# Kernel optimization log

Hardware: AMD Instinct MI355X
Metric: run time of the kernel (lower is better)

Reference implementation:

```python
import jax, jax.numpy as jnp
import numpy as np

D = 512       # d_model
DC = 768      # d_context
H = 8         # heads
DFF = 2048    # d_ff
EPS = 1e-6


def _ln(x, g, b):
    mu = jnp.mean(x, axis=-1, keepdims=True)
    var = jnp.mean(jnp.square(x - mu), axis=-1, keepdims=True)
    return (x - mu) * jax.lax.rsqrt(var + EPS) * g + b


def _mha(q_in, k_in, v_in, mask, wq, bq, wk, bk, wv, bv, wo, bo):
    # q_in [B,Sq,D], k_in/v_in [B,Sk,D], mask [B,Sq,Sk] (nonzero -> blocked)
    B, Sq, _ = q_in.shape
    Sk = k_in.shape[1]
    dh = D // H
    q = (q_in @ wq + bq).reshape(B, Sq, H, dh)
    k = (k_in @ wk + bk).reshape(B, Sk, H, dh)
    v = (v_in @ wv + bv).reshape(B, Sk, H, dh)
    scores = jnp.einsum('bqhd,bkhd->bhqk', q, k) / np.float32(np.sqrt(dh))
    scores = jnp.where(mask[:, None, :, :].astype(bool), jnp.float32(-1e18), scores)
    attn = jax.nn.softmax(scores, axis=-1)
    ctx = jnp.einsum('bhqk,bkhd->bqhd', attn, v).reshape(B, Sq, D)
    return ctx @ wo + bo


def _aggregate_chains(batch_size, ctx_out, chain_map, chain_mask):
    # ctx_out [TC,S,D]; keep positions where mask[:,:,0] is set, else -inf,
    # then max-pool chains belonging to the same example (segment max).
    keep = chain_mask[:, :, 0].astype(bool)[:, :, None]
    masked = jnp.where(keep, ctx_out, jnp.float32(-jnp.inf))
    out = jax.ops.segment_max(masked, chain_map, num_segments=batch_size)
    # replicate torch.where(out + 1 == out, 0, out): zeros out -inf entries
    return jnp.where(out + 1 == out, jnp.float32(0.0), out)


def _lin_params(key, din, dout):
    return jax.random.normal(key, (din, dout), jnp.float32) * 0.02, jnp.zeros((dout,), jnp.float32)


def setup_inputs() -> dict:
    key = jax.random.key(0)
    ks = jax.random.split(key, 20)
    B, S, TC, L = 16, 512, 128, 12
    inp = {}
    inp['inputs'] = jax.random.normal(ks[0], (B, S, D), jnp.float32)
    inp['attn_mask'] = jax.random.randint(ks[1], (B, S, S), 0, 2, jnp.int32)
    inp['chain_map'] = jax.random.randint(ks[2], (TC,), 0, B, jnp.int32)
    inp['span_embeddings'] = jax.random.normal(ks[3], (TC, L, DC), jnp.float32)
    inp['chain_mask'] = jax.random.randint(ks[4], (TC, S, L), 0, 2, jnp.int32)
    inp['ln_g'] = jnp.ones((D,), jnp.float32)
    inp['ln_b'] = jnp.zeros((D,), jnp.float32)
    inp['sa_wq'], inp['sa_bq'] = _lin_params(ks[5], D, D)
    inp['sa_wk'], inp['sa_bk'] = _lin_params(ks[6], D, D)
    inp['sa_wv'], inp['sa_bv'] = _lin_params(ks[7], D, D)
    inp['sa_wo'], inp['sa_bo'] = _lin_params(ks[8], D, D)
    inp['lc_w'], inp['lc_b'] = _lin_params(ks[9], DC, D)
    inp['ca_wq'], inp['ca_bq'] = _lin_params(ks[10], D, D)
    inp['ca_wk'], inp['ca_bk'] = _lin_params(ks[11], D, D)
    inp['ca_wv'], inp['ca_bv'] = _lin_params(ks[12], D, D)
    inp['ca_wo'], inp['ca_bo'] = _lin_params(ks[13], D, D)
    inp['g_w'], inp['g_b'] = _lin_params(ks[14], 2 * D, D)
    inp['ff_ln_g'] = jnp.ones((D,), jnp.float32)
    inp['ff_ln_b'] = jnp.zeros((D,), jnp.float32)
    inp['ff_w1'], inp['ff_b1'] = _lin_params(ks[15], D, DFF)
    inp['ff_w2'], inp['ff_b2'] = _lin_params(ks[16], DFF, D)
    return inp


def reference(inputs, attn_mask, chain_map, span_embeddings, chain_mask,
              ln_g, ln_b,
              sa_wq, sa_bq, sa_wk, sa_bk, sa_wv, sa_bv, sa_wo, sa_bo,
              lc_w, lc_b,
              ca_wq, ca_bq, ca_wk, ca_bk, ca_wv, ca_bv, ca_wo, ca_bo,
              g_w, g_b,
              ff_ln_g, ff_ln_b, ff_w1, ff_b1, ff_w2, ff_b2):
    B = inputs.shape[0]
    input_norm = _ln(inputs, ln_g, ln_b)
    attn_context = _mha(input_norm, input_norm, input_norm, attn_mask,
                        sa_wq, sa_bq, sa_wk, sa_bk, sa_wv, sa_bv, sa_wo, sa_bo)
    emb_transformed = span_embeddings @ lc_w + lc_b              # [TC,L,D]
    context_query = input_norm[chain_map]                         # [TC,S,D]
    ctx_out = _mha(context_query, emb_transformed, emb_transformed, chain_mask,
                   ca_wq, ca_bq, ca_wk, ca_bk, ca_wv, ca_bv, ca_wo, ca_bo)
    ctx_context = _aggregate_chains(B, ctx_out, chain_map, chain_mask)
    # SimpleGate
    z = jax.nn.sigmoid(jnp.concatenate((attn_context, ctx_context), axis=-1) @ g_w + g_b)
    gated = z * attn_context + (1.0 - z) * ctx_context
    out = gated + inputs  # dropout is identity at eval
    # PositionwiseFeedForward (pre-LN, residual)
    y = _ln(out, ff_ln_g, ff_ln_b)
    inter = jax.nn.relu(y @ ff_w1 + ff_b1)
    return inter @ ff_w2 + ff_b2 + out
```

## Files before the change

kernel.cpp:

```cpp
#include <hip/hip_runtime.h>
#include <hip/hip_bf16.h>
#include <math.h>

typedef float f32x4_t __attribute__((ext_vector_type(4)));
typedef __bf16 bf16x8_t __attribute__((ext_vector_type(8)));
typedef __bf16 bf16x4_t __attribute__((ext_vector_type(4)));

__device__ __forceinline__ void gload16(const void* g, void* l) {
  __builtin_amdgcn_global_load_lds((const __attribute__((address_space(1))) void*)g,
                                   (__attribute__((address_space(3))) void*)l, 16, 0, 0);
}

struct WDesc { const float* src; __bf16* hi; __bf16* lo; int K; int N; };
struct WPack { WDesc w[12]; };

__global__ __launch_bounds__(256) void prep_weights_kernel(WPack p) {
  WDesc d = p.w[blockIdx.y];
  const int tilesN = d.N >> 6;
  const int ntiles = (d.K >> 6) * tilesN;
  __shared__ float tile[64][65];
  const int tid = threadIdx.x;
  const int r = tid >> 4, cq = (tid & 15) << 2;
  const int c = tid >> 4, rq = (tid & 15) << 2;
  for (int t = blockIdx.x; t < ntiles; t += gridDim.x) {
    const int tk = t / tilesN, tn = t - tk * tilesN;
    const int k0 = tk << 6, n0 = tn << 6;
#pragma unroll
    for (int i = 0; i < 4; i++) {
      const float4 v = *reinterpret_cast<const float4*>(
          &d.src[(size_t)(k0 + r + i * 16) * d.N + n0 + cq]);
      tile[r + i * 16][cq] = v.x; tile[r + i * 16][cq + 1] = v.y;
      tile[r + i * 16][cq + 2] = v.z; tile[r + i * 16][cq + 3] = v.w;
    }
    __syncthreads();
#pragma unroll
    for (int i = 0; i < 4; i++) {
      const int cc = c + i * 16;
      const float v0 = tile[rq][cc], v1 = tile[rq + 1][cc];
      const float v2 = tile[rq + 2][cc], v3 = tile[rq + 3][cc];
      const __bf16 h0 = (__bf16)v0, h1 = (__bf16)v1, h2 = (__bf16)v2, h3 = (__bf16)v3;
      bf16x4_t hv = {h0, h1, h2, h3};
      bf16x4_t lv = {(__bf16)(v0 - (float)h0), (__bf16)(v1 - (float)h1),
                     (__bf16)(v2 - (float)h2), (__bf16)(v3 - (float)h3)};
      *reinterpret_cast<bf16x4_t*>(&d.hi[(size_t)(n0 + cc) * d.K + k0 + rq]) = hv;
      *reinterpret_cast<bf16x4_t*>(&d.lo[(size_t)(n0 + cc) * d.K + k0 + rq]) = lv;
    }
    __syncthreads();
  }
}

__global__ __launch_bounds__(256) void bias_cat_kernel(
    const float* __restrict__ b0, const float* __restrict__ b1,
    const float* __restrict__ b2, const float* __restrict__ b3,
    float* __restrict__ out) {
  const int t = blockIdx.x * 256 + threadIdx.x;
  const float* s = t < 512 ? b0 : t < 1024 ? b1 : t < 1536 ? b2 : b3;
  out[t] = s[t & 511];
}

__global__ __launch_bounds__(256) void split_kernel(
    const float* __restrict__ x, __bf16* __restrict__ h, __bf16* __restrict__ l, int nq) {
  const int i = blockIdx.x * 256 + threadIdx.x;
  if (i >= nq) return;
  const float4 v = reinterpret_cast<const float4*>(x)[i];
  const __bf16 h0 = (__bf16)v.x, h1 = (__bf16)v.y, h2 = (__bf16)v.z, h3 = (__bf16)v.w;
  bf16x4_t hv = {h0, h1, h2, h3};
  bf16x4_t lv = {(__bf16)(v.x - (float)h0), (__bf16)(v.y - (float)h1),
                 (__bf16)(v.z - (float)h2), (__bf16)(v.w - (float)h3)};
  reinterpret_cast<bf16x4_t*>(h)[i] = hv;
  reinterpret_cast<bf16x4_t*>(l)[i] = lv;
}

__global__ __launch_bounds__(256) void ln_split_kernel(
    const float* __restrict__ x, const float* __restrict__ g,
    const float* __restrict__ bb, __bf16* __restrict__ yh, __bf16* __restrict__ yl) {
  const int row = blockIdx.x * 4 + (threadIdx.x >> 6);
  const int lane = threadIdx.x & 63;
  const float* xr = x + (size_t)row * 512;
  float4 a = *reinterpret_cast<const float4*>(&xr[lane * 8]);
  float4 b4 = *reinterpret_cast<const float4*>(&xr[lane * 8 + 4]);
  float v[8] = {a.x, a.y, a.z, a.w, b4.x, b4.y, b4.z, b4.w};
  float s = 0.f;
#pragma unroll
  for (int j = 0; j < 8; j++) s += v[j];
#pragma unroll
  for (int off = 1; off < 64; off <<= 1) s += __shfl_xor(s, off);
  const float mean = s * (1.f / 512.f);
  float sq = 0.f;
#pragma unroll
  for (int j = 0; j < 8; j++) { v[j] -= mean; sq += v[j] * v[j]; }
#pragma unroll
  for (int off = 1; off < 64; off <<= 1) sq += __shfl_xor(sq, off);
  const float inv = rsqrtf(sq * (1.f / 512.f) + 1e-6f);
  bf16x8_t hv, lv;
#pragma unroll
  for (int j = 0; j < 8; j++) {
    const float o = v[j] * inv * g[lane * 8 + j] + bb[lane * 8 + j];
    const __bf16 h = (__bf16)o;
    hv[j] = h; lv[j] = (__bf16)(o - (float)h);
  }
  *reinterpret_cast<bf16x8_t*>(&yh[(size_t)row * 512 + lane * 8]) = hv;
  *reinterpret_cast<bf16x8_t*>(&yl[(size_t)row * 512 + lane * 8]) = lv;
}

template <int EPI>
__global__ __launch_bounds__(256, 2) void gemm2_kernel(
    const __bf16* __restrict__ A0h, const __bf16* __restrict__ A0l,
    const __bf16* __restrict__ A1h, const __bf16* __restrict__ A1l,
    int lda, int ksplit,
    const __bf16* __restrict__ Bh, const __bf16* __restrict__ Bl, int K,
    const float* __restrict__ bias,
    float* __restrict__ Cf, __bf16* __restrict__ Ch, __bf16* __restrict__ Cl,
    int ldc, size_t sec_stride,
    const __bf16* __restrict__ e0h, const __bf16* __restrict__ e0l,
    const __bf16* __restrict__ e1h, const __bf16* __restrict__ e1l,
    const float* __restrict__ e2) {
  __shared__ __bf16 lds[4][128][64];
  const int tid = threadIdx.x;
  const int wave = tid >> 6, lane = tid & 63;
  const int brow = blockIdx.y * 128, bcol = blockIdx.x * 128;
  const int wr = (wave >> 1) * 64, wc = (wave & 1) * 64;
  const int lr = lane & 15, hi = lane >> 4;
  const int s_row = lane >> 3;
  const int s_sc = (lane & 7) ^ s_row;
  const int tile_row = (wave < 2 ? brow : bcol) + s_row;

  f32x4_t acc[4][4] = {};

  for (int k0 = 0; k0 < K; k0 += 64) {
    const __bf16* ah = A0h; const __bf16* al = A0l; int kc = k0;
    if (k0 >= ksplit) { ah = A1h; al = A1l; kc = k0 - ksplit; }
    const __bf16* plane = wave == 0 ? ah : wave == 1 ? al : wave == 2 ? Bh : Bl;
    const int pl_lda = wave < 2 ? lda : K;
    const int pk = wave < 2 ? kc : k0;
    const __bf16* src = plane + (size_t)tile_row * pl_lda + pk + s_sc * 8;
#pragma unroll
    for (int i = 0; i < 16; i++)
      gload16(src + (size_t)i * 8 * pl_lda, &lds[wave][i * 8][0]);
    __syncthreads();
#pragma unroll
    for (int kk = 0; kk < 2; kk++) {
      bf16x8_t afh[4], afl[4], bfh[4], bfl[4];
#pragma unroll
      for (int m = 0; m < 4; m++) {
        const int row = wr + m * 16 + lr;
        const int ch = (kk * 4 + hi) ^ (row & 7);
        afh[m] = *(const bf16x8_t*)((const char*)&lds[0][0][0] + row * 128 + ch * 16);
        afl[m] = *(const bf16x8_t*)((const char*)&lds[1][0][0] + row * 128 + ch * 16);
      }
#pragma unroll
      for (int n = 0; n < 4; n++) {
        const int row = wc + n * 16 + lr;
        const int ch = (kk * 4 + hi) ^ (row & 7);
        bfh[n] = *(const bf16x8_t*)((const char*)&lds[2][0][0] + row * 128 + ch * 16);
        bfl[n] = *(const bf16x8_t*)((const char*)&lds[3][0][0] + row * 128 + ch * 16);
      }
#pragma unroll
      for (int m = 0; m < 4; m++)
#pragma unroll
        for (int n = 0; n < 4; n++) {
          acc[m][n] = __builtin_amdgcn_mfma_f32_16x16x32_bf16(afh[m], bfh[n], acc[m][n], 0, 0, 0);
          acc[m][n] = __builtin_amdgcn_mfma_f32_16x16x32_bf16(afh[m], bfl[n], acc[m][n], 0, 0, 0);
          acc[m][n] = __builtin_amdgcn_mfma_f32_16x16x32_bf16(afl[m], bfh[n], acc[m][n], 0, 0, 0);
        }
    }
    __syncthreads();
  }

#pragma unroll
  for (int m = 0; m < 4; m++) {
#pragma unroll
    for (int n = 0; n < 4; n++) {
      const int colg = bcol + wc + n * 16 + lr;
      const size_t cb = (size_t)(colg >> 9) * sec_stride + (colg & 511);
      const float bv = bias[colg];
#pragma unroll
      for (int r = 0; r < 4; r++) {
        const int row = brow + wr + m * 16 + hi * 4 + r;
        float v = acc[m][n][r] + bv;
        if constexpr (EPI == 0) {
          Cf[cb + (size_t)row * ldc] = v;
        } else if constexpr (EPI == 1) {
          const __bf16 h = (__bf16)v;
          Ch[cb + (size_t)row * ldc] = h;
          Cl[cb + (size_t)row * ldc] = (__bf16)(v - (float)h);
        } else if constexpr (EPI == 2) {
          v = fmaxf(v, 0.f);
          const __bf16 h = (__bf16)v;
          Ch[cb + (size_t)row * ldc] = h;
          Cl[cb + (size_t)row * ldc] = (__bf16)(v - (float)h);
        } else if constexpr (EPI == 3) {
          const float z = 1.f / (1.f + expf(-v));
          const size_t ei = (size_t)row * 512 + colg;
          const float a = (float)e0h[ei] + (float)e0l[ei];
          const float c = (float)e1h[ei] + (float)e1l[ei];
          Cf[cb + (size_t)row * ldc] = z * a + (1.f - z) * c + e2[ei];
        } else if constexpr (EPI == 4) {
          Cf[cb + (size_t)row * ldc] = v + e2[(size_t)row * 512 + colg];
        }
      }
    }
  }
}

__global__ __launch_bounds__(256) void sa_attn_kernel(
    const float* __restrict__ Q, const float* __restrict__ K,
    const float* __restrict__ V, const int* __restrict__ mask,
    __bf16* __restrict__ Oh, __bf16* __restrict__ Ol) {
  __shared__ float qs[64][67];
  __shared__ float ks[64][67];
  __shared__ float vs[64][67];
  const int tid = threadIdx.x;
  const int b = blockIdx.z, h = blockIdx.y, q0 = blockIdx.x * 64;
  const int ty = tid >> 4, tx = tid & 15;
#pragma unroll
  for (int i = 0; i < 4; i++) {
    const int fi = i * 256 + tid;
    const int r = fi >> 4, dq = (fi & 15) << 2;
    const float4 v = *reinterpret_cast<const float4*>(&Q[((size_t)(b * 512 + q0 + r)) * 512 + h * 64 + dq]);
    qs[r][dq] = v.x; qs[r][dq + 1] = v.y; qs[r][dq + 2] = v.z; qs[r][dq + 3] = v.w;
  }
  float m[4], l[4], o[4][4];
#pragma unroll
  for (int i = 0; i < 4; i++) {
    m[i] = -INFINITY; l[i] = 0.f;
#pragma unroll
    for (int j = 0; j < 4; j++) o[i][j] = 0.f;
  }
  for (int kt = 0; kt < 8; kt++) {
    const int k0 = kt * 64;
    __syncthreads();
#pragma unroll
    for (int i = 0; i < 4; i++) {
      const int fi = i * 256 + tid;
      const int r = fi >> 4, dq = (fi & 15) << 2;
      const float4 kv = *reinterpret_cast<const float4*>(&K[((size_t)(b * 512 + k0 + r)) * 512 + h * 64 + dq]);
      ks[r][dq] = kv.x; ks[r][dq + 1] = kv.y; ks[r][dq + 2] = kv.z; ks[r][dq + 3] = kv.w;
      const float4 vv = *reinterpret_cast<const float4*>(&V[((size_t)(b * 512 + k0 + r)) * 512 + h * 64 + dq]);
      vs[r][dq] = vv.x; vs[r][dq + 1] = vv.y; vs[r][dq + 2] = vv.z; vs[r][dq + 3] = vv.w;
    }
    __syncthreads();
    float s[4][4] = {};
#pragma unroll 8
    for (int d = 0; d < 64; d++) {
      float qv[4], kv[4];
#pragma unroll
      for (int i = 0; i < 4; i++) qv[i] = qs[ty * 4 + i][d];
#pragma unroll
      for (int j = 0; j < 4; j++) kv[j] = ks[tx * 4 + j][d];
#pragma unroll
      for (int i = 0; i < 4; i++)
#pragma unroll
        for (int j = 0; j < 4; j++) s[i][j] += qv[i] * kv[j];
    }
    float scale[4];
#pragma unroll
    for (int i = 0; i < 4; i++) {
      const int qi = q0 + ty * 4 + i;
      const int4 mv = *reinterpret_cast<const int4*>(&mask[((size_t)b * 512 + qi) * 512 + k0 + tx * 4]);
      s[i][0] = mv.x ? -1e18f : s[i][0] * 0.125f;
      s[i][1] = mv.y ? -1e18f : s[i][1] * 0.125f;
      s[i][2] = mv.z ? -1e18f : s[i][2] * 0.125f;
      s[i][3] = mv.w ? -1e18f : s[i][3] * 0.125f;
      float mx = fmaxf(fmaxf(s[i][0], s[i][1]), fmaxf(s[i][2], s[i][3]));
#pragma unroll
      for (int off = 1; off <= 8; off <<= 1) mx = fmaxf(mx, __shfl_xor(mx, off));
      const float mnew = fmaxf(m[i], mx);
      float rs = 0.f;
#pragma unroll
      for (int j = 0; j < 4; j++) { const float p = expf(s[i][j] - mnew); s[i][j] = p; rs += p; }
#pragma unroll
      for (int off = 1; off <= 8; off <<= 1) rs += __shfl_xor(rs, off);
      scale[i] = expf(m[i] - mnew);
      l[i] = l[i] * scale[i] + rs;
      m[i] = mnew;
    }
    __syncthreads();
#pragma unroll
    for (int i = 0; i < 4; i++)
#pragma unroll
      for (int j = 0; j < 4; j++) ks[ty * 4 + i][tx * 4 + j] = s[i][j];
#pragma unroll
    for (int i = 0; i < 4; i++)
#pragma unroll
      for (int j = 0; j < 4; j++) o[i][j] *= scale[i];
    __syncthreads();
#pragma unroll 8
    for (int kk = 0; kk < 64; kk++) {
      float pv[4], vv[4];
#pragma unroll
      for (int i = 0; i < 4; i++) pv[i] = ks[ty * 4 + i][kk];
#pragma unroll
      for (int j = 0; j < 4; j++) vv[j] = vs[kk][tx * 4 + j];
#pragma unroll
      for (int i = 0; i < 4; i++)
#pragma unroll
        for (int j = 0; j < 4; j++) o[i][j] += pv[i] * vv[j];
    }
  }
#pragma unroll
  for (int i = 0; i < 4; i++) {
    const float inv = 1.f / l[i];
    const size_t base = ((size_t)(b * 512 + q0 + ty * 4 + i)) * 512 + h * 64 + tx * 4;
    bf16x4_t hv, lv;
#pragma unroll
    for (int j = 0; j < 4; j++) {
      const float ov = o[i][j] * inv;
      const __bf16 hh = (__bf16)ov;
      hv[j] = hh; lv[j] = (__bf16)(ov - (float)hh);
    }
    *reinterpret_cast<bf16x4_t*>(&Oh[base]) = hv;
    *reinterpret_cast<bf16x4_t*>(&Ol[base]) = lv;
  }
}

__global__ __launch_bounds__(256) void ca_attn_kernel(
    const float* __restrict__ Qbase, const float* __restrict__ Kc,
    const float* __restrict__ Vc, const int* __restrict__ chain_map,
    const int* __restrict__ chain_mask,
    __bf16* __restrict__ Oh, __bf16* __restrict__ Ol, int c0) {
  __shared__ float ks[12][512];
  __shared__ float vs[12][512];
  const int tid = threadIdx.x;
  const int cl = blockIdx.y, c = c0 + cl, s0 = blockIdx.x * 32;
#pragma unroll
  for (int i = 0; i < 6; i++) {
    const int fi = i * 256 + tid;
    const int lrow = fi >> 7, dq = (fi & 127) << 2;
    *reinterpret_cast<float4*>(&ks[lrow][dq]) =
        *reinterpret_cast<const float4*>(&Kc[((size_t)c * 12 + lrow) * 512 + dq]);
    *reinterpret_cast<float4*>(&vs[lrow][dq]) =
        *reinterpret_cast<const float4*>(&Vc[((size_t)c * 12 + lrow) * 512 + dq]);
  }
  __syncthreads();
  const int h = tid >> 5, sl = tid & 31;
  const int s = s0 + sl;
  const int bq = chain_map[c];
  const float* qrow = &Qbase[((size_t)(bq * 512 + s)) * 512 + h * 64];
  float4 q4[16];
#pragma unroll
  for (int i = 0; i < 16; i++) q4[i] = *reinterpret_cast<const float4*>(&qrow[i * 4]);
  const int* mrow = &chain_mask[((size_t)(c * 512 + s)) * 12];
  float sc[12];
  float mx = -INFINITY;
#pragma unroll
  for (int lI = 0; lI < 12; lI++) {
    float acc = 0.f;
#pragma unroll
    for (int i = 0; i < 16; i++) {
      const float4 kv = *reinterpret_cast<const float4*>(&ks[lI][h * 64 + i * 4]);
      acc += q4[i].x * kv.x + q4[i].y * kv.y + q4[i].z * kv.z + q4[i].w * kv.w;
    }
    acc *= 0.125f;
    if (mrow[lI]) acc = -1e18f;
    sc[lI] = acc;
    mx = fmaxf(mx, acc);
  }
  float sum = 0.f;
#pragma unroll
  for (int lI = 0; lI < 12; lI++) { sc[lI] = expf(sc[lI] - mx); sum += sc[lI]; }
  const float inv = 1.f / sum;
  const size_t obase = ((size_t)(cl * 512 + s)) * 512 + h * 64;
#pragma unroll
  for (int dq = 0; dq < 16; dq++) {
    float4 ov = make_float4(0.f, 0.f, 0.f, 0.f);
#pragma unroll
    for (int lI = 0; lI < 12; lI++) {
      const float4 vv = *reinterpret_cast<const float4*>(&vs[lI][h * 64 + dq * 4]);
      ov.x += sc[lI] * vv.x; ov.y += sc[lI] * vv.y;
      ov.z += sc[lI] * vv.z; ov.w += sc[lI] * vv.w;
    }
    float vo[4] = {ov.x * inv, ov.y * inv, ov.z * inv, ov.w * inv};
    bf16x4_t hv, lv;
#pragma unroll
    for (int j = 0; j < 4; j++) {
      const __bf16 hh = (__bf16)vo[j];
      hv[j] = hh; lv[j] = (__bf16)(vo[j] - (float)hh);
    }
    *reinterpret_cast<bf16x4_t*>(&Oh[obase + dq * 4]) = hv;
    *reinterpret_cast<bf16x4_t*>(&Ol[obase + dq * 4]) = lv;
  }
}

template <int MODE>
__global__ __launch_bounds__(256) void agg2_kernel(
    const float* __restrict__ ctxB, const int* __restrict__ chain_map,
    const int* __restrict__ chain_mask,
    __bf16* __restrict__ ch, __bf16* __restrict__ cl, int c0) {
  const int s = blockIdx.x, b = blockIdx.y, tid = threadIdx.x;
  const size_t orow = ((size_t)(b * 512 + s)) * 512;
  float v0 = -3.0e38f, v1 = -3.0e38f;
  if (MODE != 0) {
    v0 = (float)ch[orow + tid] + (float)cl[orow + tid];
    v1 = (float)ch[orow + 256 + tid] + (float)cl[orow + 256 + tid];
  }
  for (int i = 0; i < 16; i++) {
    const int c = c0 + i;
    if (chain_map[c] == b && chain_mask[((size_t)(c * 512 + s)) * 12] != 0) {
      const float* row = &ctxB[((size_t)(i * 512 + s)) * 512];
      v0 = fmaxf(v0, row[tid]);
      v1 = fmaxf(v1, row[tid + 256]);
    }
  }
  if (MODE == 2) {
    if (v0 < -1.0e38f) v0 = 0.f;
    if (v1 < -1.0e38f) v1 = 0.f;
  }
  const __bf16 h0 = (__bf16)v0, h1 = (__bf16)v1;
  ch[orow + tid] = h0;        cl[orow + tid] = (__bf16)(v0 - (float)h0);
  ch[orow + 256 + tid] = h1;  cl[orow + 256 + tid] = (__bf16)(v1 - (float)h1);
}

extern "C" void kernel_launch(void* const* d_in, const int* in_sizes, int n_in,
                              void* d_out, int out_size, void* d_ws, size_t ws_size,
                              hipStream_t stream) {
  const float* inputs     = (const float*)d_in[0];
  const int*   attn_mask  = (const int*)d_in[1];
  const int*   chain_map  = (const int*)d_in[2];
  const float* span       = (const float*)d_in[3];
  const int*   chain_mask = (const int*)d_in[4];
  const float* ln_g = (const float*)d_in[5];
  const float* ln_b = (const float*)d_in[6];
  const float* sa_bq = (const float*)d_in[8];
  const float* sa_bk = (const float*)d_in[10];
  const float* sa_bv = (const float*)d_in[12];
  const float* sa_bo = (const float*)d_in[14];
  const float* lc_b  = (const float*)d_in[16];
  const float* ca_bq = (const float*)d_in[18];
  const float* ca_bk = (const float*)d_in[20];
  const float* ca_bv = (const float*)d_in[22];
  const float* ca_bo = (const float*)d_in[24];
  const float* g_b   = (const float*)d_in[26];
  const float* ff_ln_g = (const float*)d_in[27];
  const float* ff_ln_b = (const float*)d_in[28];
  const float* ff_b1 = (const float*)d_in[30];
  const float* ff_b2 = (const float*)d_in[32];

  char* ws = (char*)d_ws;
  size_t off = 0;
  auto alloc = [&](size_t bytes) -> void* {
    off = (off + 255) & ~(size_t)255;
    void* p = ws + off;
    off += bytes;
    return p;
  };

  const size_t wel[9] = {2048ull*512, 768ull*512, 512ull*512, 512ull*512,
                         512ull*512, 512ull*512, 1024ull*512, 512ull*2048, 2048ull*512};
  __bf16* WH[9]; __bf16* WL[9];
  for (int i = 0; i < 9; i++) {
    WH[i] = (__bf16*)alloc(wel[i] * 2);
    WL[i] = (__bf16*)alloc(wel[i] * 2);
  }
  WPack pack;
  pack.w[0] = {(const float*)d_in[7],  WH[0],               WL[0],               512, 512};
  pack.w[1] = {(const float*)d_in[9],  WH[0] + 512*512,     WL[0] + 512*512,     512, 512};
  pack.w[2] = {(const float*)d_in[11], WH[0] + 1024*512,    WL[0] + 1024*512,    512, 512};
  pack.w[3] = {(const float*)d_in[17], WH[0] + 1536*512,    WL[0] + 1536*512,    512, 512};
  pack.w[4] = {(const float*)d_in[15], WH[1], WL[1], 768, 512};
  pack.w[5] = {(const float*)d_in[19], WH[2], WL[2], 512, 512};
  pack.w[6] = {(const float*)d_in[21], WH[3], WL[3], 512, 512};
  pack.w[7] = {(const float*)d_in[13], WH[4], WL[4], 512, 512};
  pack.w[8] = {(const float*)d_in[23], WH[5], WL[5], 512, 512};
  pack.w[9] = {(const float*)d_in[25], WH[6], WL[6], 1024, 512};
  pack.w[10] = {(const float*)d_in[29], WH[7], WL[7], 512, 2048};
  pack.w[11] = {(const float*)d_in[31], WH[8], WL[8], 2048, 512};

  float* bias_cat = (float*)alloc(2048 * 4);

  const size_t E_BSD = 8192ull * 512;
  char* R_A = (char*)alloc(E_BSD * 4);
  char* R_B = (char*)alloc(E_BSD * 16);
  __bf16* spanh = (__bf16*)alloc(1536ull * 768 * 2);
  __bf16* spanl = (__bf16*)alloc(1536ull * 768 * 2);
  __bf16* embh  = (__bf16*)alloc(1536ull * 512 * 2);
  __bf16* embl  = (__bf16*)alloc(1536ull * 512 * 2);
  float*  v_ca  = (float*)alloc(1536ull * 512 * 4);
  if (ws_size < off) return;

  __bf16* xh = (__bf16*)R_A;           __bf16* xl = xh + E_BSD;
  __bf16* sh = xh;                     __bf16* sl = xl;
  __bf16* cah = xh;                    __bf16* cal = xl;
  float*  out1 = (float*)R_A;
  float* QKVQ = (float*)R_B;
  float* saQ = QKVQ;
  float* saK = QKVQ + E_BSD;
  float* saV = QKVQ + 2 * E_BSD;
  float* caQ = QKVQ + 3 * E_BSD;
  float*  ctxB  = (float*)R_B;
  __bf16* ah_pl = (__bf16*)(R_B + E_BSD * 4);
  __bf16* al_pl = ah_pl + E_BSD;
  __bf16* cth   = (__bf16*)(R_B + E_BSD * 8);
  __bf16* ctl   = cth + E_BSD;
  __bf16* yh    = (__bf16*)(R_B + E_BSD * 12);
  __bf16* yl    = yh + E_BSD;
  __bf16* ih    = (__bf16*)R_B;
  __bf16* il    = ih + 4096ull * 2048;
  float* k_ca = (float*)spanh;
  float* dout = (float*)d_out;
  const int KBIG = 1 << 30;
  const float* Z = nullptr;
  const __bf16* ZB = nullptr;

  auto gemm = [&](int EPI, const __bf16* a0h, const __bf16* a0l,
                  const __bf16* a1h, const __bf16* a1l, int lda, int ksplit,
                  int wi, int K, const float* bias,
                  float* cf, __bf16* chp, __bf16* clp, int ldc, size_t secs,
                  const __bf16* E0h, const __bf16* E0l,
                  const __bf16* E1h, const __bf16* E1l, const float* E2,
                  int M, int N) {
    dim3 grid(N / 128, M / 128);
    switch (EPI) {
      case 0: gemm2_kernel<0><<<grid, 256, 0, stream>>>(a0h, a0l, a1h, a1l, lda, ksplit, WH[wi], WL[wi], K, bias, cf, chp, clp, ldc, secs, E0h, E0l, E1h, E1l, E2); break;
      case 1: gemm2_kernel<1><<<grid, 256, 0, stream>>>(a0h, a0l, a1h, a1l, lda, ksplit, WH[wi], WL[wi], K, bias, cf, chp, clp, ldc, secs, E0h, E0l, E1h, E1l, E2); break;
      case 2: gemm2_kernel<2><<<grid, 256, 0, stream>>>(a0h, a0l, a1h, a1l, lda, ksplit, WH[wi], WL[wi], K, bias, cf, chp, clp, ldc, secs, E0h, E0l, E1h, E1l, E2); break;
      case 3: gemm2_kernel<3><<<grid, 256, 0, stream>>>(a0h, a0l, a1h, a1l, lda, ksplit, WH[wi], WL[wi], K, bias, cf, chp, clp, ldc, secs, E0h, E0l, E1h, E1l, E2); break;
      case 4: gemm2_kernel<4><<<grid, 256, 0, stream>>>(a0h, a0l, a1h, a1l, lda, ksplit, WH[wi], WL[wi], K, bias, cf, chp, clp, ldc, secs, E0h, E0l, E1h, E1l, E2); break;
    }
  };

  prep_weights_kernel<<<dim3(64, 12), 256, 0, stream>>>(pack);
  bias_cat_kernel<<<8, 256, 0, stream>>>(sa_bq, sa_bk, sa_bv, ca_bq, bias_cat);
  split_kernel<<<1152, 256, 0, stream>>>(span, spanh, spanl, 1536 * 768 / 4);
  ln_split_kernel<<<2048, 256, 0, stream>>>(inputs, ln_g, ln_b, xh, xl);

  gemm(0, xh, xl, xh, xl, 512, KBIG, 0, 512, bias_cat,
       QKVQ, nullptr, nullptr, 512, (size_t)E_BSD,
       ZB, ZB, ZB, ZB, Z, 8192, 2048);

  sa_attn_kernel<<<dim3(8, 8, 16), 256, 0, stream>>>(saQ, saK, saV, attn_mask, sh, sl);
  gemm(1, sh, sl, sh, sl, 512, KBIG, 4, 512, sa_bo,
       nullptr, ah_pl, al_pl, 512, 0, ZB, ZB, ZB, ZB, Z, 8192, 512);

  gemm(1, spanh, spanl, spanh, spanl, 768, KBIG, 1, 768, lc_b,
       nullptr, embh, embl, 512, 0, ZB, ZB, ZB, ZB, Z, 1536, 512);
  gemm(0, embh, embl, embh, embl, 512, KBIG, 2, 512, ca_bk,
       k_ca, nullptr, nullptr, 512, 0, ZB, ZB, ZB, ZB, Z, 1536, 512);
  gemm(0, embh, embl, embh, embl, 512, KBIG, 3, 512, ca_bv,
       v_ca, nullptr, nullptr, 512, 0, ZB, ZB, ZB, ZB, Z, 1536, 512);

  for (int chk = 0; chk < 8; chk++) {
    const int c0 = chk * 16;
    ca_attn_kernel<<<dim3(16, 16), 256, 0, stream>>>(caQ, k_ca, v_ca, chain_map, chain_mask, cah, cal, c0);
    gemm(0, cah, cal, cah, cal, 512, KBIG, 5, 512, ca_bo,
         ctxB, nullptr, nullptr, 512, 0, ZB, ZB, ZB, ZB, Z, 8192, 512);
    if (chk == 0)      agg2_kernel<0><<<dim3(512, 16), 256, 0, stream>>>(ctxB, chain_map, chain_mask, cth, ctl, c0);
    else if (chk == 7) agg2_kernel<2><<<dim3(512, 16), 256, 0, stream>>>(ctxB, chain_map, chain_mask, cth, ctl, c0);
    else               agg2_kernel<1><<<dim3(512, 16), 256, 0, stream>>>(ctxB, chain_map, chain_mask, cth, ctl, c0);
  }

  gemm(3, ah_pl, al_pl, cth, ctl, 512, 512, 6, 1024, g_b,
       out1, nullptr, nullptr, 512, 0, ah_pl, al_pl, cth, ctl, inputs, 8192, 512);

  ln_split_kernel<<<2048, 256, 0, stream>>>(out1, ff_ln_g, ff_ln_b, yh, yl);
  for (int r0 = 0; r0 < 8192; r0 += 4096) {
    gemm(2, yh + (size_t)r0 * 512, yl + (size_t)r0 * 512,
         yh + (size_t)r0 * 512, yl + (size_t)r0 * 512, 512, KBIG, 7, 512, ff_b1,
         nullptr, ih, il, 2048, 512, ZB, ZB, ZB, ZB, Z, 4096, 2048);
    gemm(4, ih, il, ih, il, 2048, KBIG, 8, 2048, ff_b2,
         dout + (size_t)r0 * 512, nullptr, nullptr, 512, 0,
         ZB, ZB, ZB, ZB, out1 + (size_t)r0 * 512, 4096, 512);
  }
}
```

Baseline: 1.196 ms.

## Move self-attention to bf16x3 MFMA with split hi/lo Q/K/V from QKV GEMM

The self-attention kernel now runs QK^T and PV on MFMA using a three-product hi/lo bf16 split instead of scalar fp32 FMAs in LDS. To feed it, the QKV projection GEMM gets a new epilogue that writes Q and K as bf16 hi/lo planes and V transposed per head. Cross-attention Q stays fp32. The aim is to cut the attention compute cost on matrix cores. It adds scattered transposed stores in the GEMM epilogue and relies on the hi/lo split to keep accuracy close to fp32.

```diff
diff --git a/kernel.cpp b/kernel.cpp
--- a/kernel.cpp
+++ b/kernel.cpp
@@ -111,6 +111,8 @@
     const __bf16* __restrict__ Bh, const __bf16* __restrict__ Bl, int K,
     const float* __restrict__ bias,
     float* __restrict__ Cf, __bf16* __restrict__ Ch, __bf16* __restrict__ Cl,
+    __bf16* __restrict__ C2h, __bf16* __restrict__ C2l,
+    __bf16* __restrict__ C3h, __bf16* __restrict__ C3l,
     int ldc, size_t sec_stride,
     const __bf16* __restrict__ e0h, const __bf16* __restrict__ e0l,
     const __bf16* __restrict__ e1h, const __bf16* __restrict__ e1l,
@@ -197,120 +199,163 @@
           Cf[cb + (size_t)row * ldc] = z * a + (1.f - z) * c + e2[ei];
         } else if constexpr (EPI == 4) {
           Cf[cb + (size_t)row * ldc] = v + e2[(size_t)row * 512 + colg];
+        } else if constexpr (EPI == 5) {
+          const int sec = colg >> 9, cc = colg & 511;
+          const __bf16 h = (__bf16)v;
+          const __bf16 lo = (__bf16)(v - (float)h);
+          if (sec == 0)      { Ch[(size_t)row * 512 + cc] = h;  Cl[(size_t)row * 512 + cc] = lo; }
+          else if (sec == 1) { C2h[(size_t)row * 512 + cc] = h; C2l[(size_t)row * 512 + cc] = lo; }
+          else if (sec == 2) {
+            const int bb2 = row >> 9, ss = row & 511, hh2 = cc >> 6, dv = cc & 63;
+            const size_t va = ((size_t)((bb2 * 8 + hh2) * 64 + dv)) * 512 + ss;
+            C3h[va] = h; C3l[va] = lo;
+          } else {
+            Cf[(size_t)row * 512 + cc] = v;
+          }
         }
       }
     }
   }
 }
 
-__global__ __launch_bounds__(256) void sa_attn_kernel(
-    const float* __restrict__ Q, const float* __restrict__ K,
-    const float* __restrict__ V, const int* __restrict__ mask,
+__global__ __launch_bounds__(256, 2) void sa_attn_mfma_kernel(
+    const __bf16* __restrict__ Qh_g, const __bf16* __restrict__ Ql_g,
+    const __bf16* __restrict__ Kh_g, const __bf16* __restrict__ Kl_g,
+    const __bf16* __restrict__ Vth_g, const __bf16* __restrict__ Vtl_g,
+    const int* __restrict__ mask,
     __bf16* __restrict__ Oh, __bf16* __restrict__ Ol) {
-  __shared__ float qs[64][67];
-  __shared__ float ks[64][67];
-  __shared__ float vs[64][67];
+  __shared__ __bf16 Qs[2][64][64];
+  __shared__ __bf16 Ks[2][64][64];
+  __shared__ __bf16 Vs[2][64][64];
+  __shared__ __bf16 Ps[2][64][64];
   const int tid = threadIdx.x;
-  const int b = blockIdx.z, h = blockIdx.y, q0 = blockIdx.x * 64;
-  const int ty = tid >> 4, tx = tid & 15;
-#pragma unroll
-  for (int i = 0; i < 4; i++) {
-    const int fi = i * 256 + tid;
-    const int r = fi >> 4, dq = (fi & 15) << 2;
-    const float4 v = *reinterpret_cast<const float4*>(&Q[((size_t)(b * 512 + q0 + r)) * 512 + h * 64 + dq]);
-    qs[r][dq] = v.x; qs[r][dq + 1] = v.y; qs[r][dq + 2] = v.z; qs[r][dq + 3] = v.w;
-  }
-  float m[4], l[4], o[4][4];
-#pragma unroll
-  for (int i = 0; i < 4; i++) {
-    m[i] = -INFINITY; l[i] = 0.f;
-#pragma unroll
-    for (int j = 0; j < 4; j++) o[i][j] = 0.f;
-  }
+  const int wid = tid >> 6, lane = tid & 63;
+  const int q0 = blockIdx.x * 64;
+  const int h = blockIdx.y, b = blockIdx.z;
+  const int lr = lane & 15, hi = lane >> 4;
+  const int s_row = lane >> 3;
+  const int s_sc = (lane & 7) ^ s_row;
+
+  {
+    const __bf16* qp = (wid < 2 ? Qh_g : Ql_g);
+    const int pl = (wid < 2 ? 0 : 1);
+    const int r0 = (wid & 1) * 32;
+    const __bf16* src = qp + (size_t)(b * 512 + q0 + r0 + s_row) * 512 + h * 64 + s_sc * 8;
+#pragma unroll
+    for (int i = 0; i < 4; i++)
+      gload16(src + (size_t)i * 8 * 512, &Qs[pl][r0 + i * 8][0]);
+  }
+  f32x4_t accO[4] = {};
+  float m_[4], l_[4];
+#pragma unroll
+  for (int j = 0; j < 4; j++) { m_[j] = -INFINITY; l_[j] = 0.f; }
+
   for (int kt = 0; kt < 8; kt++) {
     const int k0 = kt * 64;
     __syncthreads();
-#pragma unroll
-    for (int i = 0; i < 4; i++) {
-      const int fi = i * 256 + tid;
-      const int r = fi >> 4, dq = (fi & 15) << 2;
-      const float4 kv = *reinterpret_cast<const float4*>(&K[((size_t)(b * 512 + k0 + r)) * 512 + h * 64 + dq]);
-      ks[r][dq] = kv.x; ks[r][dq + 1] = kv.y; ks[r][dq + 2] = kv.z; ks[r][dq + 3] = kv.w;
-      const float4 vv = *reinterpret_cast<const float4*>(&V[((size_t)(b * 512 + k0 + r)) * 512 + h * 64 + dq]);
-      vs[r][dq] = vv.x; vs[r][dq + 1] = vv.y; vs[r][dq + 2] = vv.z; vs[r][dq + 3] = vv.w;
+    {
+      const __bf16* plane = wid == 0 ? Kh_g : wid == 1 ? Kl_g : wid == 2 ? Vth_g : Vtl_g;
+      size_t srow; int scol;
+      if (wid < 2) { srow = (size_t)(b * 512 + k0 + s_row);          scol = h * 64; }
+      else         { srow = (size_t)((b * 8 + h) * 64 + s_row);      scol = k0; }
+      const __bf16* src = plane + srow * 512 + scol + s_sc * 8;
+      __bf16* dst0 = (wid == 0) ? &Ks[0][0][0] : (wid == 1) ? &Ks[1][0][0]
+                   : (wid == 2) ? &Vs[0][0][0] : &Vs[1][0][0];
+#pragma unroll
+      for (int i = 0; i < 8; i++)
+        gload16(src + (size_t)i * 8 * 512, dst0 + i * 8 * 64);
     }
     __syncthreads();
-    float s[4][4] = {};
-#pragma unroll 8
-    for (int d = 0; d < 64; d++) {
-      float qv[4], kv[4];
-#pragma unroll
-      for (int i = 0; i < 4; i++) qv[i] = qs[ty * 4 + i][d];
-#pragma unroll
-      for (int j = 0; j < 4; j++) kv[j] = ks[tx * 4 + j][d];
-#pragma unroll
-      for (int i = 0; i < 4; i++)
-#pragma unroll
-        for (int j = 0; j < 4; j++) s[i][j] += qv[i] * kv[j];
-    }
-    float scale[4];
-#pragma unroll
-    for (int i = 0; i < 4; i++) {
-      const int qi = q0 + ty * 4 + i;
-      const int4 mv = *reinterpret_cast<const int4*>(&mask[((size_t)b * 512 + qi) * 512 + k0 + tx * 4]);
-      s[i][0] = mv.x ? -1e18f : s[i][0] * 0.125f;
-      s[i][1] = mv.y ? -1e18f : s[i][1] * 0.125f;
-      s[i][2] = mv.z ? -1e18f : s[i][2] * 0.125f;
-      s[i][3] = mv.w ? -1e18f : s[i][3] * 0.125f;
-      float mx = fmaxf(fmaxf(s[i][0], s[i][1]), fmaxf(s[i][2], s[i][3]));
-#pragma unroll
-      for (int off = 1; off <= 8; off <<= 1) mx = fmaxf(mx, __shfl_xor(mx, off));
-      const float mnew = fmaxf(m[i], mx);
+
+    f32x4_t acc[4] = {};
+#pragma unroll
+    for (int kk = 0; kk < 2; kk++) {
+      const int arow = wid * 16 + lr;
+      const int ach = (kk * 4 + hi) ^ (arow & 7);
+      bf16x8_t aqh = *(const bf16x8_t*)&Qs[0][arow][ach * 8];
+      bf16x8_t aql = *(const bf16x8_t*)&Qs[1][arow][ach * 8];
+#pragma unroll
+      for (int n = 0; n < 4; n++) {
+        const int brw = n * 16 + lr;
+        const int bch = (kk * 4 + hi) ^ (brw & 7);
+        bf16x8_t bkh = *(const bf16x8_t*)&Ks[0][brw][bch * 8];
+        bf16x8_t bkl = *(const bf16x8_t*)&Ks[1][brw][bch * 8];
+        acc[n] = __builtin_amdgcn_mfma_f32_16x16x32_bf16(aqh, bkh, acc[n], 0, 0, 0);
+        acc[n] = __builtin_amdgcn_mfma_f32_16x16x32_bf16(aqh, bkl, acc[n], 0, 0, 0);
+        acc[n] = __builtin_amdgcn_mfma_f32_16x16x32_bf16(aql, bkh, acc[n], 0, 0, 0);
+      }
+    }
+
+    float p[4][4];
+    const int qbase = b * 512 + q0 + wid * 16 + hi * 4;
+#pragma unroll
+    for (int j = 0; j < 4; j++) {
+      float rowmax = -INFINITY;
+#pragma unroll
+      for (int n = 0; n < 4; n++) {
+        const int mk = mask[(size_t)(qbase + j) * 512 + k0 + n * 16 + lr];
+        const float sv = mk ? -1e18f : acc[n][j] * 0.125f;
+        p[n][j] = sv;
+        rowmax = fmaxf(rowmax, sv);
+      }
+#pragma unroll
+      for (int off = 1; off <= 8; off <<= 1) rowmax = fmaxf(rowmax, __shfl_xor(rowmax, off));
+      const float mnew = fmaxf(m_[j], rowmax);
+      const float scale = expf(m_[j] - mnew);
       float rs = 0.f;
 #pragma unroll
-      for (int j = 0; j < 4; j++) { const float p = expf(s[i][j] - mnew); s[i][j] = p; rs += p; }
+      for (int n = 0; n < 4; n++) { const float e = expf(p[n][j] - mnew); p[n][j] = e; rs += e; }
 #pragma unroll
       for (int off = 1; off <= 8; off <<= 1) rs += __shfl_xor(rs, off);
-      scale[i] = expf(m[i] - mnew);
-      l[i] = l[i] * scale[i] + rs;
-      m[i] = mnew;
-    }
-    __syncthreads();
-#pragma unroll
-    for (int i = 0; i < 4; i++)
-#pragma unroll
-      for (int j = 0; j < 4; j++) ks[ty * 4 + i][tx * 4 + j] = s[i][j];
-#pragma unroll
-    for (int i = 0; i < 4; i++)
-#pragma unroll
-      for (int j = 0; j < 4; j++) o[i][j] *= scale[i];
-    __syncthreads();
-#pragma unroll 8
-    for (int kk = 0; kk < 64; kk++) {
-      float pv[4], vv[4];
-#pragma unroll
-      for (int i = 0; i < 4; i++) pv[i] = ks[ty * 4 + i][kk];
-#pragma unroll
-      for (int j = 0; j < 4; j++) vv[j] = vs[kk][tx * 4 + j];
-#pragma unroll
-      for (int i = 0; i < 4; i++)
-#pragma unroll
-        for (int j = 0; j < 4; j++) o[i][j] += pv[i] * vv[j];
-    }
-  }
-#pragma unroll
-  for (int i = 0; i < 4; i++) {
-    const float inv = 1.f / l[i];
-    const size_t base = ((size_t)(b * 512 + q0 + ty * 4 + i)) * 512 + h * 64 + tx * 4;
-    bf16x4_t hv, lv;
+      l_[j] = l_[j] * scale + rs;
+      m_[j] = mnew;
+#pragma unroll
+      for (int nv = 0; nv < 4; nv++) accO[nv][j] *= scale;
+    }
+
 #pragma unroll
     for (int j = 0; j < 4; j++) {
-      const float ov = o[i][j] * inv;
-      const __bf16 hh = (__bf16)ov;
-      hv[j] = hh; lv[j] = (__bf16)(ov - (float)hh);
-    }
-    *reinterpret_cast<bf16x4_t*>(&Oh[base]) = hv;
-    *reinterpret_cast<bf16x4_t*>(&Ol[base]) = lv;
+      const int qrow = wid * 16 + hi * 4 + j;
+#pragma unroll
+      for (int n = 0; n < 4; n++) {
+        const int col = n * 16 + lr;
+        const int colp = ((((col >> 3) ^ (qrow & 7)) << 3) | (col & 7));
+        const __bf16 ph = (__bf16)p[n][j];
+        Ps[0][qrow][colp] = ph;
+        Ps[1][qrow][colp] = (__bf16)(p[n][j] - (float)ph);
+      }
+    }
+
+#pragma unroll
+    for (int kk = 0; kk < 2; kk++) {
+      const int arow = wid * 16 + lr;
+      const int ach = (kk * 4 + hi) ^ (arow & 7);
+      bf16x8_t aph = *(const bf16x8_t*)&Ps[0][arow][ach * 8];
+      bf16x8_t apl = *(const bf16x8_t*)&Ps[1][arow][ach * 8];
+#pragma unroll
+      for (int nv = 0; nv < 4; nv++) {
+        const int brw = nv * 16 + lr;
+        const int bch = (kk * 4 + hi) ^ (brw & 7);
+        bf16x8_t bvh = *(const bf16x8_t*)&Vs[0][brw][bch * 8];
+        bf16x8_t bvl = *(const bf16x8_t*)&Vs[1][brw][bch * 8];
+        accO[nv] = __builtin_amdgcn_mfma_f32_16x16x32_bf16(aph, bvh, accO[nv], 0, 0, 0);
+        accO[nv] = __builtin_amdgcn_mfma_f32_16x16x32_bf16(aph, bvl, accO[nv], 0, 0, 0);
+        accO[nv] = __builtin_amdgcn_mfma_f32_16x16x32_bf16(apl, bvh, accO[nv], 0, 0, 0);
+      }
+    }
+  }
+
+#pragma unroll
+  for (int j = 0; j < 4; j++) {
+    const float inv = 1.f / l_[j];
+    const size_t orow = (size_t)(b * 512 + q0 + wid * 16 + hi * 4 + j) * 512 + h * 64;
+#pragma unroll
+    for (int nv = 0; nv < 4; nv++) {
+      const float o = accO[nv][j] * inv;
+      const __bf16 hh = (__bf16)o;
+      Oh[orow + nv * 16 + lr] = hh;
+      Ol[orow + nv * 16 + lr] = (__bf16)(o - (float)hh);
+    }
   }
 }
 
@@ -482,40 +527,39 @@
   __bf16* sh = xh;                     __bf16* sl = xl;
   __bf16* cah = xh;                    __bf16* cal = xl;
   float*  out1 = (float*)R_A;
-  float* QKVQ = (float*)R_B;
-  float* saQ = QKVQ;
-  float* saK = QKVQ + E_BSD;
-  float* saV = QKVQ + 2 * E_BSD;
-  float* caQ = QKVQ + 3 * E_BSD;
+  __bf16* Qh_g = (__bf16*)R_B;                    __bf16* Ql_g = Qh_g + E_BSD;
+  __bf16* Kh_g = (__bf16*)(R_B + E_BSD * 4);      __bf16* Kl_g = Kh_g + E_BSD;
+  __bf16* VTh_g = (__bf16*)(R_B + E_BSD * 8);     __bf16* VTl_g = VTh_g + E_BSD;
+  float*  caQ  = (float*)(R_B + E_BSD * 12);
   float*  ctxB  = (float*)R_B;
-  __bf16* ah_pl = (__bf16*)(R_B + E_BSD * 4);
-  __bf16* al_pl = ah_pl + E_BSD;
-  __bf16* cth   = (__bf16*)(R_B + E_BSD * 8);
-  __bf16* ctl   = cth + E_BSD;
-  __bf16* yh    = (__bf16*)(R_B + E_BSD * 12);
-  __bf16* yl    = yh + E_BSD;
-  __bf16* ih    = (__bf16*)R_B;
-  __bf16* il    = ih + 4096ull * 2048;
+  __bf16* ah_pl = (__bf16*)(R_B + E_BSD * 4);     __bf16* al_pl = ah_pl + E_BSD;
+  __bf16* cth   = (__bf16*)(R_B + E_BSD * 8);     __bf16* ctl   = cth + E_BSD;
+  __bf16* yh    = (__bf16*)(R_B + E_BSD * 12);    __bf16* yl    = yh + E_BSD;
+  __bf16* ih    = (__bf16*)R_B;                   __bf16* il    = ih + 4096ull * 2048;
   float* k_ca = (float*)spanh;
   float* dout = (float*)d_out;
   const int KBIG = 1 << 30;
   const float* Z = nullptr;
   const __bf16* ZB = nullptr;
+  __bf16* ZM = nullptr;
 
   auto gemm = [&](int EPI, const __bf16* a0h, const __bf16* a0l,
                   const __bf16* a1h, const __bf16* a1l, int lda, int ksplit,
                   int wi, int K, const float* bias,
-                  float* cf, __bf16* chp, __bf16* clp, int ldc, size_t secs,
+                  float* cf, __bf16* chp, __bf16* clp,
+                  __bf16* c2h, __bf16* c2l, __bf16* c3h, __bf16* c3l,
+                  int ldc, size_t secs,
                   const __bf16* E0h, const __bf16* E0l,
                   const __bf16* E1h, const __bf16* E1l, const float* E2,
                   int M, int N) {
     dim3 grid(N / 128, M / 128);
     switch (EPI) {
-      case 0: gemm2_kernel<0><<<grid, 256, 0, stream>>>(a0h, a0l, a1h, a1l, lda, ksplit, WH[wi], WL[wi], K, bias, cf, chp, clp, ldc, secs, E0h, E0l, E1h, E1l, E2); break;
-      case 1: gemm2_kernel<1><<<grid, 256, 0, stream>>>(a0h, a0l, a1h, a1l, lda, ksplit, WH[wi], WL[wi], K, bias, cf, chp, clp, ldc, secs, E0h, E0l, E1h, E1l, E2); break;
-      case 2: gemm2_kernel<2><<<grid, 256, 0, stream>>>(a0h, a0l, a1h, a1l, lda, ksplit, WH[wi], WL[wi], K, bias, cf, chp, clp, ldc, secs, E0h, E0l, E1h, E1l, E2); break;
-      case 3: gemm2_kernel<3><<<grid, 256, 0, stream>>>(a0h, a0l, a1h, a1l, lda, ksplit, WH[wi], WL[wi], K, bias, cf, chp, clp, ldc, secs, E0h, E0l, E1h, E1l, E2); break;
-      case 4: gemm2_kernel<4><<<grid, 256, 0, stream>>>(a0h, a0l, a1h, a1l, lda, ksplit, WH[wi], WL[wi], K, bias, cf, chp, clp, ldc, secs, E0h, E0l, E1h, E1l, E2); break;
+      case 0: gemm2_kernel<0><<<grid, 256, 0, stream>>>(a0h, a0l, a1h, a1l, lda, ksplit, WH[wi], WL[wi], K, bias, cf, chp, clp, c2h, c2l, c3h, c3l, ldc, secs, E0h, E0l, E1h, E1l, E2); break;
+      case 1: gemm2_kernel<1><<<grid, 256, 0, stream>>>(a0h, a0l, a1h, a1l, lda, ksplit, WH[wi], WL[wi], K, bias, cf, chp, clp, c2h, c2l, c3h, c3l, ldc, secs, E0h, E0l, E1h, E1l, E2); break;
+      case 2: gemm2_kernel<2><<<grid, 256, 0, stream>>>(a0h, a0l, a1h, a1l, lda, ksplit, WH[wi], WL[wi], K, bias, cf, chp, clp, c2h, c2l, c3h, c3l, ldc, secs, E0h, E0l, E1h, E1l, E2); break;
+      case 3: gemm2_kernel<3><<<grid, 256, 0, stream>>>(a0h, a0l, a1h, a1l, lda, ksplit, WH[wi], WL[wi], K, bias, cf, chp, clp, c2h, c2l, c3h, c3l, ldc, secs, E0h, E0l, E1h, E1l, E2); break;
+      case 4: gemm2_kernel<4><<<grid, 256, 0, stream>>>(a0h, a0l, a1h, a1l, lda, ksplit, WH[wi], WL[wi], K, bias, cf, chp, clp, c2h, c2l, c3h, c3l, ldc, secs, E0h, E0l, E1h, E1l, E2); break;
+      case 5: gemm2_kernel<5><<<grid, 256, 0, stream>>>(a0h, a0l, a1h, a1l, lda, ksplit, WH[wi], WL[wi], K, bias, cf, chp, clp, c2h, c2l, c3h, c3l, ldc, secs, E0h, E0l, E1h, E1l, E2); break;
     }
   };
 
@@ -524,41 +568,43 @@
   split_kernel<<<1152, 256, 0, stream>>>(span, spanh, spanl, 1536 * 768 / 4);
   ln_split_kernel<<<2048, 256, 0, stream>>>(inputs, ln_g, ln_b, xh, xl);
 
-  gemm(0, xh, xl, xh, xl, 512, KBIG, 0, 512, bias_cat,
-       QKVQ, nullptr, nullptr, 512, (size_t)E_BSD,
+  gemm(5, xh, xl, xh, xl, 512, KBIG, 0, 512, bias_cat,
+       caQ, Qh_g, Ql_g, Kh_g, Kl_g, VTh_g, VTl_g, 512, 0,
        ZB, ZB, ZB, ZB, Z, 8192, 2048);
 
-  sa_attn_kernel<<<dim3(8, 8, 16), 256, 0, stream>>>(saQ, saK, saV, attn_mask, sh, sl);
+  sa_attn_mfma_kernel<<<dim3(8, 8, 16), 256, 0, stream>>>(
+      Qh_g, Ql_g, Kh_g, Kl_g, VTh_g, VTl_g, attn_mask, sh, sl);
   gemm(1, sh, sl, sh, sl, 512, KBIG, 4, 512, sa_bo,
-       nullptr, ah_pl, al_pl, 512, 0, ZB, ZB, ZB, ZB, Z, 8192, 512);
+       nullptr, ah_pl, al_pl, ZM, ZM, ZM, ZM, 512, 0, ZB, ZB, ZB, ZB, Z, 8192, 512);
 
   gemm(1, spanh, spanl, spanh, spanl, 768, KBIG, 1, 768, lc_b,
-       nullptr, embh, embl, 512, 0, ZB, ZB, ZB, ZB, Z, 1536, 512);
+       nullptr, embh, embl, ZM, ZM, ZM, ZM, 512, 0, ZB, ZB, ZB, ZB, Z, 1536, 512);
   gemm(0, embh, embl, embh, embl, 512, KBIG, 2, 512, ca_bk,
-       k_ca, nullptr, nullptr, 512, 0, ZB, ZB, ZB, ZB, Z, 1536, 512);
+       k_ca, nullptr, nullptr, ZM, ZM, ZM, ZM, 512, 0, ZB, ZB, ZB, ZB, Z, 1536, 512);
   gemm(0, embh, embl, embh, embl, 512, KBIG, 3, 512, ca_bv,
-       v_ca, nullptr, nullptr, 512, 0, ZB, ZB, ZB, ZB, Z, 1536, 512);
+       v_ca, nullptr, nullptr, ZM, ZM, ZM, ZM, 512, 0, ZB, ZB, ZB, ZB, Z, 1536, 512);
 
   for (int chk = 0; chk < 8; chk++) {
     const int c0 = chk * 16;
     ca_attn_kernel<<<dim3(16, 16), 256, 0, stream>>>(caQ, k_ca, v_ca, chain_map, chain_mask, cah, cal, c0);
     gemm(0, cah, cal, cah, cal, 512, KBIG, 5, 512, ca_bo,
-         ctxB, nullptr, nullptr, 512, 0, ZB, ZB, ZB, ZB, Z, 8192, 512);
+         ctxB, nullptr, nullptr, ZM, ZM, ZM, ZM, 512, 0, ZB, ZB, ZB, ZB, Z, 8192, 512);
     if (chk == 0)      agg2_kernel<0><<<dim3(512, 16), 256, 0, stream>>>(ctxB, chain_map, chain_mask, cth, ctl, c0);
     else if (chk == 7) agg2_kernel<2><<<dim3(512, 16), 256, 0, stream>>>(ctxB, chain_map, chain_mask, cth, ctl, c0);
     else               agg2_kernel<1><<<dim3(512, 16), 256, 0, stream>>>(ctxB, chain_map, chain_mask, cth, ctl, c0);
   }
 
   gemm(3, ah_pl, al_pl, cth, ctl, 512, 512, 6, 1024, g_b,
-       out1, nullptr, nullptr, 512, 0, ah_pl, al_pl, cth, ctl, inputs, 8192, 512);
+       out1, nullptr, nullptr, ZM, ZM, ZM, ZM, 512, 0,
+       ah_pl, al_pl, cth, ctl, inputs, 8192, 512);
 
   ln_split_kernel<<<2048, 256, 0, stream>>>(out1, ff_ln_g, ff_ln_b, yh, yl);
   for (int r0 = 0; r0 < 8192; r0 += 4096) {
     gemm(2, yh + (size_t)r0 * 512, yl + (size_t)r0 * 512,
          yh + (size_t)r0 * 512, yl + (size_t)r0 * 512, 512, KBIG, 7, 512, ff_b1,
-         nullptr, ih, il, 2048, 512, ZB, ZB, ZB, ZB, Z, 4096, 2048);
+         nullptr, ih, il, ZM, ZM, ZM, ZM, 2048, 512, ZB, ZB, ZB, ZB, Z, 4096, 2048);
     gemm(4, ih, il, ih, il, 2048, KBIG, 8, 2048, ff_b2,
-         dout + (size_t)r0 * 512, nullptr, nullptr, 512, 0,
+         dout + (size_t)r0 * 512, nullptr, nullptr, ZM, ZM, ZM, ZM, 512, 0,
          ZB, ZB, ZB, ZB, out1 + (size_t)r0 * 512, 4096, 512);
   }
 }
```

New measurement: 1.196 ms. No clear change (-0.1%).
